# Kernel tuning notes

Measured on AMD Instinct MI355X. Metric: run time of the kernel, lower is better.

## Reference

```python
import jax, jax.numpy as jnp
import numpy as np
from jax import lax

B0 = 64
WIN, STEP, WSIZE, NCH, T = 5, 50, 100, 59, 300
EPS = 1e-5


def _bn(y, g, b, axes):
    mu = y.mean(axis=axes, keepdims=True)
    var = y.var(axis=axes, keepdims=True)
    return (y - mu) * lax.rsqrt(var + EPS) * g + b


def _conv_block(x, w, b, g, be, pad):
    # Conv2d(1->20, (1,kw), padding='same') + BN + LeakyReLU + AvgPool(1,2)
    y = lax.conv_general_dilated(x, w, (1, 1), [(0, 0), (pad, pad)],
                                 dimension_numbers=('NCHW', 'OIHW', 'NCHW'))
    y = y + b[None, :, None, None]
    y = _bn(y, g[None, :, None, None], be[None, :, None, None], (0, 2, 3))
    y = jax.nn.leaky_relu(y, 0.01)
    n, c, h, w_ = y.shape
    return y[..., :(w_ // 2) * 2].reshape(n, c, h, w_ // 2, 2).mean(-1)


def _lstm(xs, Wih, Whh, bih, bhh):
    # torch LSTM gate order: i, f, g, o
    Bn, H = xs.shape[0], Whh.shape[1]
    bb = bih + bhh

    def step(carry, xt):
        h, c = carry
        gates = xt @ Wih.T + h @ Whh.T + bb
        i, f, g, o = jnp.split(gates, 4, axis=-1)
        c = jax.nn.sigmoid(f) * c + jax.nn.sigmoid(i) * jnp.tanh(g)
        h = jax.nn.sigmoid(o) * jnp.tanh(c)
        return (h, c), h

    init = (jnp.zeros((Bn, H), xs.dtype), jnp.zeros((Bn, H), xs.dtype))
    (h, _), ys = lax.scan(step, init, xs.transpose(1, 0, 2))
    return ys.transpose(1, 0, 2), h


def _forward(x, w1, b1, g1, be1, w2, b2, g2, be2, w3, b3, g3, be3,
             w13, b13, g13, be13, gcn_w, gcn_b, edge_w, bn2_g, bn2_b,
             w11, b11, wih0, whh0, bih0, bhh0, wih1, whh1, bih1, bhh1,
             edge_index, batch_size):
    B = batch_size
    N = B * NCH
    # segment 300 samples into 5 overlapping windows of 100 (step 50)
    xr = x.reshape(B, NCH, -1).transpose(0, 2, 1)              # [B,T,59]
    idx = (jnp.arange(WIN) * STEP)[:, None] + jnp.arange(WSIZE)[None, :]
    seg = xr[:, idx, :]                                        # [B,5,100,59]
    xc = seg.transpose(0, 1, 3, 2).reshape(B * WIN, 1, NCH, WSIZE)
    # three parallel temporal conv branches
    x1 = _conv_block(xc, w1, b1, g1, be1, 62)
    x2 = _conv_block(xc, w2, b2, g2, be2, 29)
    x3 = _conv_block(xc, w3, b3, g3, be3, 15)
    xcat = jnp.concatenate([x1, x2, x3], axis=-1)              # [B*5,20,59,150]
    # cnn_13: 1x1 conv + BN + LeakyReLU, then channel sum
    y = jnp.einsum('nchw,oc->nohw', xcat, w13[:, :, 0, 0]) + b13[None, :, None, None]
    y = _bn(y, g13[None, :, None, None], be13[None, :, None, None], (0, 2, 3))
    y = jax.nn.leaky_relu(y, 0.01)
    feat = y.sum(axis=1).reshape(B, WIN, NCH, -1).transpose(0, 2, 1, 3).reshape(N, WIN, -1)  # [N,5,150]
    # GCNConv with relu'd learned per-edge weight, applied to all 5 windows
    row, col = edge_index[0], edge_index[1]
    ew = jnp.tile(jax.nn.relu(edge_w), B)                      # [E_total]
    h = jnp.einsum('nwf,fo->nwo', feat, gcn_w)                 # [N,5,100]
    deg = jnp.zeros((N,), h.dtype).at[col].add(ew) + 1.0       # +1 = self-loop weight
    dinv = lax.rsqrt(deg)
    nrm = dinv[row] * ew * dinv[col]
    agg = jnp.zeros_like(h).at[col].add(h[row] * nrm[:, None, None])
    agg = agg + h * (dinv * dinv)[:, None, None] + gcn_b       # self-loop + bias
    gout = _bn(agg, bn2_g, bn2_b, (0,))                        # per-window BN over nodes
    # cnn_11: Conv2d(1->10,(59,2)) + LeakyReLU + AvgPool(1,2)
    z = gout.reshape(B, NCH, WIN, -1).transpose(0, 2, 1, 3).reshape(B * WIN, 1, NCH, -1)
    y2 = lax.conv_general_dilated(z, w11, (1, 1), [(0, 0), (0, 0)],
                                  dimension_numbers=('NCHW', 'OIHW', 'NCHW'))
    y2 = jax.nn.leaky_relu(y2 + b11[None, :, None, None], 0.01)  # [B*5,10,1,99]
    n, c, hh, ww = y2.shape
    y2 = y2[..., :(ww // 2) * 2].reshape(n, c, hh, ww // 2, 2).mean(-1)
    seq = y2.reshape(B, WIN, -1)                               # [B,5,490]
    out1, _ = _lstm(seq, wih0, whh0, bih0, bhh0)
    out2, hlast = _lstm(out1, wih1, whh1, bih1, bhh1)
    attn = jax.nn.softmax(jnp.einsum('bth,bh->bt', out2, hlast), axis=1)
    return jnp.einsum('bth,bt->bh', out2, attn)                # [B,256]


def setup_inputs():
    key = jax.random.key(0)
    ks = jax.random.split(key, 24)
    B, E = B0, 216
    N = B * NCH
    x = jax.random.normal(ks[0], (N, T), jnp.float32)
    src = jax.random.randint(ks[1], (E,), 0, NCH)
    dst = jax.random.randint(ks[2], (E,), 0, NCH)
    off = (jnp.arange(B) * NCH)[:, None]
    edge_index = jnp.stack([(src[None, :] + off).reshape(-1),
                            (dst[None, :] + off).reshape(-1)]).astype(jnp.int32)
    s = 0.05
    return {
        'x': x,
        'w1': jax.random.normal(ks[3], (20, 1, 1, 125)) * s, 'b1': jnp.zeros(20), 'g1': jnp.ones(20), 'be1': jnp.zeros(20),
        'w2': jax.random.normal(ks[4], (20, 1, 1, 59)) * s, 'b2': jnp.zeros(20), 'g2': jnp.ones(20), 'be2': jnp.zeros(20),
        'w3': jax.random.normal(ks[5], (20, 1, 1, 31)) * s, 'b3': jnp.zeros(20), 'g3': jnp.ones(20), 'be3': jnp.zeros(20),
        'w13': jax.random.normal(ks[6], (10, 20, 1, 1)) * s, 'b13': jnp.zeros(10), 'g13': jnp.ones(10), 'be13': jnp.zeros(10),
        'gcn_w': jax.random.normal(ks[7], (150, 100)) * 0.08, 'gcn_b': jnp.zeros(100),
        'edge_w': jax.random.normal(ks[8], (216,)),
        'bn2_g': jnp.ones(100), 'bn2_b': jnp.zeros(100),
        'w11': jax.random.normal(ks[9], (10, 1, 59, 2)) * s, 'b11': jnp.zeros(10),
        'wih0': jax.random.normal(ks[10], (1024, 490)) * 0.04, 'whh0': jax.random.normal(ks[11], (1024, 256)) * 0.06,
        'bih0': jnp.zeros(1024), 'bhh0': jnp.zeros(1024),
        'wih1': jax.random.normal(ks[12], (1024, 256)) * 0.06, 'whh1': jax.random.normal(ks[13], (1024, 256)) * 0.06,
        'bih1': jnp.zeros(1024), 'bhh1': jnp.zeros(1024),
        'edge_index': edge_index,
        'batch_size': B,
    }


def reference(x, w1, b1, g1, be1, w2, b2, g2, be2, w3, b3, g3, be3,
              w13, b13, g13, be13, gcn_w, gcn_b, edge_w, bn2_g, bn2_b,
              w11, b11, wih0, whh0, bih0, bhh0, wih1, whh1, bih1, bhh1,
              edge_index, batch_size):
    return _forward(x, w1, b1, g1, be1, w2, b2, g2, be2, w3, b3, g3, be3,
                    w13, b13, g13, be13, gcn_w, gcn_b, edge_w, bn2_g, bn2_b,
                    w11, b11, wih0, whh0, bih0, bhh0, wih1, whh1, bih1, bhh1,
                    edge_index, batch_size)
```

## Files before the change

### kernel.cpp

```cpp
#include <hip/hip_runtime.h>
#include <math.h>

#define EPS 1e-5f

constexpr int NCH  = 59;
constexpr int T_   = 300;
constexpr int WIN  = 5;
constexpr int WSIZE= 100;
constexpr int Bb   = 64;
constexpr int NB   = Bb*WIN;
constexpr int NN   = Bb*NCH;
constexpr int EW_N = 216;
constexpr int NE   = EW_N*Bb;
constexpr int C1   = 20;
constexpr int C13  = 10;
constexpr int F150 = 150;
constexpr int F100 = 100;
constexpr int HID  = 256;
constexpr int GATES= 1024;
constexpr int NROW = NB*NCH;
constexpr int NWIN = NROW;
constexpr float CNT1  = 1888000.0f;
constexpr float CNT13 = 2832000.0f;

__device__ __forceinline__ float leaky(float v){ return v >= 0.f ? v : 0.01f*v; }
__device__ __forceinline__ float sigm(float v){ return 1.f/(1.f+expf(-v)); }

__global__ __launch_bounds__(256)
void zero_kernel(float* __restrict__ p, int n)
{
    int i = blockIdx.x*256 + threadIdx.x;
    if (i < n) p[i] = 0.f;
}

__global__ __launch_bounds__(256)
void syrk_kernel(const float* __restrict__ x, float* __restrict__ M, float* __restrict__ V)
{
    __shared__ float xs[128*100 + 16];
    const int k0 = blockIdx.x * 128;
    const int tid = threadIdx.x;
    for (int i = tid; i < 128*100; i += 256){
        int wl = i / 100, u = i - wl*100;
        int w = k0 + wl;
        float v = 0.f;
        if (w < NWIN){
            int row = w / 5, win = w - row*5;
            v = x[(size_t)row*T_ + win*50 + u];
        }
        xs[i] = v;
    }
    if (tid < 16) xs[128*100 + tid] = 0.f;
    __syncthreads();
    if (tid < 100){
        float s = 0.f;
        for (int kk = 0; kk < 128; kk++) s += xs[kk*100 + tid];
        atomicAdd(&V[tid], s);
    }
    const int i = tid >> 4, j = tid & 15;
    float acc[7][7];
    #pragma unroll
    for (int a=0;a<7;a++)
        #pragma unroll
        for (int b=0;b<7;b++) acc[a][b]=0.f;
    for (int kk = 0; kk < 128; kk++){
        const float* xr = &xs[kk*100];
        float xu[7], xv[7];
        #pragma unroll
        for (int a=0;a<7;a++) xu[a] = xr[a*16 + i];
        #pragma unroll
        for (int b=0;b<7;b++) xv[b] = xr[b*16 + j];
        #pragma unroll
        for (int a=0;a<7;a++)
            #pragma unroll
            for (int b=0;b<7;b++) acc[a][b] += xu[a]*xv[b];
    }
    #pragma unroll
    for (int a=0;a<7;a++){
        int u = a*16 + i;
        if (u < 100){
            #pragma unroll
            for (int b=0;b<7;b++){
                int v = b*16 + j;
                if (v < 100) atomicAdd(&M[u*100 + v], acc[a][b]);
            }
        }
    }
}

__global__ void qprep_kernel(const float* __restrict__ M, const float* __restrict__ V,
                             float* __restrict__ Q, float* __restrict__ R)
{
    int d = threadIdx.x;
    if (d < 100){
        float s = 0.f;
        Q[d*101] = 0.f;
        for (int t = 1; t <= 100; t++){
            int u = t - 1;
            if (u + d < 100) s += M[u*100 + u + d];
            Q[d*101 + t] = s;
        }
    } else if (d == 100){
        float s = 0.f;
        R[0] = 0.f;
        for (int t = 1; t <= 100; t++){ s += V[t-1]; R[t] = s; }
    }
}

__global__ __launch_bounds__(256)
void gram_finalize(const float* __restrict__ Q, const float* __restrict__ Rg,
                   const float* __restrict__ w1, const float* __restrict__ w2, const float* __restrict__ w3,
                   const float* __restrict__ g1, const float* __restrict__ be1,
                   const float* __restrict__ g2, const float* __restrict__ be2,
                   const float* __restrict__ g3, const float* __restrict__ be3,
                   float* __restrict__ sclall, float* __restrict__ sftall)
{
    __shared__ float Qs[100*101];
    __shared__ float ws[128];
    __shared__ float Rs[104];
    __shared__ float red[8];
    const int conv = blockIdx.x / 20, c = blockIdx.x - conv*20;
    const int KW  = conv==0 ? 125 : (conv==1 ? 59 : 31);
    const int PAD = (KW-1)/2;
    const float* wt = conv==0 ? w1 : (conv==1 ? w2 : w3);
    const int tid = threadIdx.x;
    for (int i = tid; i < 100*101; i += 256) Qs[i] = Q[i];
    for (int i = tid; i < KW; i += 256) ws[i] = wt[c*KW + i];
    if (tid < 101) Rs[tid] = Rg[tid];
    __syncthreads();
    const int DMAX = KW < 100 ? KW : 100;
    float sq = 0.f;
    for (int d = 0; d < DMAX; d++){
        float fac = (d == 0) ? 1.f : 2.f;
        for (int k1 = tid; k1 < KW - d; k1 += 256){
            int lo = k1 - PAD; if (lo < 0) lo = 0;
            int hi = 100 - d; int h2 = 100 + k1 - PAD; if (h2 < hi) hi = h2;
            if (hi > lo) sq += fac * ws[k1]*ws[k1+d] * (Qs[d*101 + hi] - Qs[d*101 + lo]);
        }
    }
    float sm = 0.f;
    for (int k = tid; k < KW; k += 256){
        int lo = k - PAD; if (lo < 0) lo = 0;
        int hi = 100; int h2 = k - PAD + 100; if (h2 < hi) hi = h2;
        if (hi > lo) sm += ws[k]*(Rs[hi] - Rs[lo]);
    }
    for (int off = 32; off; off >>= 1){
        sq += __shfl_down(sq, off, 64);
        sm += __shfl_down(sm, off, 64);
    }
    int wave = tid >> 6, lane = tid & 63;
    if (lane == 0){ red[wave] = sq; red[4+wave] = sm; }
    __syncthreads();
    if (tid == 0){
        float q = (red[0]+red[1]+red[2]+red[3]) / CNT1;
        float m = (red[4]+red[5]+red[6]+red[7]) / CNT1;
        float var = q - m*m;
        float rs = rsqrtf(var + EPS);
        const float* g  = conv==0 ? g1  : (conv==1 ? g2  : g3);
        const float* be = conv==0 ? be1 : (conv==1 ? be2 : be3);
        sclall[conv*C1 + c] = rs*g[c];
        sftall[conv*C1 + c] = be[c] - m*rs*g[c];
    }
}

template<int KW, int PAD, int CIDX>
__global__ __launch_bounds__(256)
void conv1d_apply(const float* __restrict__ x, const float* __restrict__ wt_g,
                  const float* __restrict__ sclall, const float* __restrict__ sftall,
                  const float* __restrict__ w13,
                  float* __restrict__ stats13, float* __restrict__ y13)
{
    __shared__ float xp[WIN*240];
    __shared__ float lstat[2*C13];

    const int row = blockIdx.x;
    const int b   = row / NCH, hh = row - b*NCH;
    const int tid = threadIdx.x;
    const float* xrow = x + (size_t)row*T_;

    for (int i = tid; i < WIN*240; i += 256){
        int win = i/240, ii = i - win*240;
        int t = ii - PAD;
        xp[i] = (t >= 0 && t < WSIZE) ? xrow[win*50 + t] : 0.f;
    }
    if (tid < 2*C13) lstat[tid] = 0.f;
    __syncthreads();

    const bool active = (tid < 250);
    const int win = tid / 50, u = tid - win*50;

    float a0[C1], a1[C1];
    #pragma unroll
    for (int c = 0; c < C1; c++){ a0[c] = 0.f; a1[c] = 0.f; }

    if (active){
        const float* xw = &xp[win*240 + 2*u];
        float xa = xw[0];
        #pragma unroll 4
        for (int k = 0; k < KW; k++){
            float xb = xw[k+1];
            #pragma unroll
            for (int c = 0; c < C1; c++){
                float wv = wt_g[c*KW + k];
                a0[c] += wv*xa;
                a1[c] += wv*xb;
            }
            xa = xb;
        }
    }

    float y[C13];
    if (active){
        float pooled[C1];
        #pragma unroll
        for (int c = 0; c < C1; c++){
            float sc = sclall[CIDX*C1 + c];
            float sf = sftall[CIDX*C1 + c];
            pooled[c] = 0.5f*(leaky(a0[c]*sc + sf) + leaky(a1[c]*sc + sf));
        }
        #pragma unroll
        for (int o = 0; o < C13; o++){
            float acc = 0.f;
            #pragma unroll
            for (int c = 0; c < C1; c++) acc += w13[o*C1 + c]*pooled[c];
            y[o] = acc;
        }
        const int n = b*WIN + win;
        #pragma unroll
        for (int o = 0; o < C13; o++)
            y13[(((size_t)n*C13 + o)*NCH + hh)*F150 + CIDX*50 + u] = y[o];
    } else {
        #pragma unroll
        for (int o = 0; o < C13; o++) y[o] = 0.f;
    }
    #pragma unroll
    for (int o = 0; o < C13; o++){
        float s = y[o], q = y[o]*y[o];
        for (int off = 32; off; off >>= 1){
            s += __shfl_down(s, off, 64);
            q += __shfl_down(q, off, 64);
        }
        if ((tid & 63) == 0){
            atomicAdd(&lstat[o],       s);
            atomicAdd(&lstat[C13 + o], q);
        }
    }
    __syncthreads();
    const int st = row & 63;
    if (tid < 2*C13) atomicAdd(&stats13[st*(2*C13) + tid], lstat[tid]);
}

__global__ void finalize_bn13(const float* __restrict__ stats13,
                              const float* __restrict__ g13, const float* __restrict__ be13,
                              float* __restrict__ scl13, float* __restrict__ sft13)
{
    int o = threadIdx.x;
    if (o >= C13) return;
    float s=0.f, q=0.f;
    for (int st=0; st<64; st++){
        s += stats13[st*20 + o];
        q += stats13[st*20 + C13 + o];
    }
    float m = s/CNT13, v = q/CNT13 - m*m;
    float rs = rsqrtf(v + EPS);
    scl13[o] = rs*g13[o];
    sft13[o] = be13[o] - m*rs*g13[o];
}

__global__ __launch_bounds__(256)
void feat_kernel(const float* __restrict__ y13,
                 const float* __restrict__ scl13, const float* __restrict__ sft13,
                 float* __restrict__ feat)
{
    __shared__ float scl[C13], sft[C13];
    int blk = blockIdx.x;
    int n = blk / NCH, hh = blk - n*NCH;
    int b = n / WIN, win = n - b*WIN;
    int tid = threadIdx.x;
    if (tid < C13){ scl[tid] = scl13[tid]; sft[tid] = sft13[tid]; }
    __syncthreads();
    float* fr = feat + ((size_t)(b*NCH+hh)*WIN + win)*F150;
    for (int f = tid; f < F150; f += 256){
        float acc = 0.f;
        #pragma unroll
        for (int o = 0; o < C13; o++){
            float v = y13[((size_t)(n*C13+o)*NCH+hh)*F150 + f];
            acc += leaky(v*scl[o] + sft[o]);
        }
        fr[f] = acc;
    }
}

__global__ __launch_bounds__(256)
void gcn_h_kernel(const float* __restrict__ feat, const float* __restrict__ gw,
                  float* __restrict__ h)
{
    __shared__ float fr[8*F150];
    int r0 = blockIdx.x*8;
    int tid = threadIdx.x;
    for (int i = tid; i < 8*F150; i += 256) fr[i] = feat[(size_t)r0*F150 + i];
    __syncthreads();
    for (int idx = tid; idx < 8*F100; idx += 256){
        int rr = idx / F100, j = idx - rr*F100;
        float acc = 0.f;
        const float* f = &fr[rr*F150];
        for (int k = 0; k < F150; k++) acc += f[k]*gw[k*F100 + j];
        h[(size_t)(r0+rr)*F100 + j] = acc;
    }
}

__global__ void deg_kernel(const int* __restrict__ ei, const float* __restrict__ ew,
                           float* __restrict__ deg)
{
    int e = blockIdx.x*blockDim.x + threadIdx.x;
    if (e >= NE) return;
    int c = ei[NE + e];
    float w = ew[e % EW_N]; w = w > 0.f ? w : 0.f;
    atomicAdd(&deg[c], w);
}

__global__ void dinv_kernel(float* __restrict__ deg)
{
    int i = blockIdx.x*blockDim.x + threadIdx.x;
    if (i < NN) deg[i] = rsqrtf(deg[i] + 1.0f);
}

__global__ __launch_bounds__(64)
void agg_kernel(const int* __restrict__ ei, const float* __restrict__ ew,
                const float* __restrict__ dinv, const float* __restrict__ h,
                float* __restrict__ agg)
{
    int e = blockIdx.x;
    int r = ei[e], c = ei[NE + e];
    float w = ew[e % EW_N]; w = w > 0.f ? w : 0.f;
    float nrm = dinv[r]*w*dinv[c];
    const float* hr = h + (size_t)r*(WIN*F100);
    float* ac = agg + (size_t)c*(WIN*F100);
    for (int i = threadIdx.x; i < WIN*F100; i += 64)
        atomicAdd(&ac[i], hr[i]*nrm);
}

__global__ __launch_bounds__(256)
void bn2_stats_kernel(const float* __restrict__ h, const float* __restrict__ dinv,
                      float* __restrict__ agg, float* __restrict__ s2sum, float* __restrict__ s2sq)
{
    int tid = threadIdx.x;
    int c0 = tid, c1 = tid + 256;
    float s0=0.f,q0=0.f,s1=0.f,q1=0.f;
    for (int rr = 0; rr < NCH; rr++){
        int node = blockIdx.x*NCH + rr;
        float d = dinv[node]; float d2 = d*d;
        const float* hr = h + (size_t)node*(WIN*F100);
        float* ar = agg + (size_t)node*(WIN*F100);
        float v0 = ar[c0] + hr[c0]*d2;
        ar[c0] = v0; s0 += v0; q0 += v0*v0;
        if (c1 < WIN*F100){
            float v1 = ar[c1] + hr[c1]*d2;
            ar[c1] = v1; s1 += v1; q1 += v1*v1;
        }
    }
    atomicAdd(&s2sum[c0], s0); atomicAdd(&s2sq[c0], q0);
    if (c1 < WIN*F100){ atomicAdd(&s2sum[c1], s1); atomicAdd(&s2sq[c1], q1); }
}

__global__ void bn2_fin_kernel(const float* __restrict__ s2sum, const float* __restrict__ s2sq,
                               const float* __restrict__ g2, const float* __restrict__ b2,
                               float* __restrict__ scl2, float* __restrict__ sft2)
{
    int c = blockIdx.x*blockDim.x + threadIdx.x;
    if (c >= WIN*F100) return;
    int f = c % F100;
    float m = s2sum[c]/(float)NN;
    float v = s2sq[c]/(float)NN - m*m;
    float rs = rsqrtf(v + EPS);
    scl2[c] = rs*g2[f];
    sft2[c] = b2[f] - m*rs*g2[f];
}

__global__ __launch_bounds__(256)
void zconv_kernel(const float* __restrict__ agg,
                  const float* __restrict__ scl2, const float* __restrict__ sft2,
                  const float* __restrict__ w11, const float* __restrict__ b11,
                  float* __restrict__ seq)
{
    __shared__ float z[NCH*WSIZE];
    __shared__ float ws[C13*NCH*2];
    __shared__ float sc[WSIZE], sf[WSIZE];
    int n = blockIdx.x;
    int b = n / WIN, win = n - b*WIN;
    int tid = threadIdx.x;
    if (tid < WSIZE){ sc[tid] = scl2[win*F100 + tid]; sf[tid] = sft2[win*F100 + tid]; }
    for (int i = tid; i < C13*NCH*2; i += 256) ws[i] = w11[i];
    __syncthreads();
    for (int i = tid; i < NCH*WSIZE; i += 256){
        int ch = i / WSIZE, t = i - ch*WSIZE;
        int node = b*NCH + ch;
        float v = agg[(size_t)node*(WIN*F100) + win*F100 + t];
        z[i] = v*sc[t] + sf[t];
    }
    __syncthreads();
    float* sq = seq + (size_t)n*490;
    for (int idx = tid; idx < C13*49; idx += 256){
        int o = idx / 49, p = idx - o*49;
        float ve = b11[o], vo = b11[o];
        const float* wo = &ws[o*NCH*2];
        for (int ch = 0; ch < NCH; ch++){
            float z0 = z[ch*WSIZE + 2*p];
            float z1 = z[ch*WSIZE + 2*p + 1];
            float z2 = z[ch*WSIZE + 2*p + 2];
            float w0 = wo[ch*2], w1 = wo[ch*2 + 1];
            ve += w0*z0 + w1*z1;
            vo += w0*z1 + w1*z2;
        }
        sq[o*49 + p] = 0.5f*(leaky(ve) + leaky(vo));
    }
}

__global__ void transpose_kernel(const float* __restrict__ src, float* __restrict__ dst, int R, int C)
{
    int idx = blockIdx.x*blockDim.x + threadIdx.x;
    if (idx >= R*C) return;
    int r = idx % R, c = idx / R;
    dst[idx] = src[(size_t)r*C + c];
}

__global__ __launch_bounds__(512)
void xgates_kernel(const float* __restrict__ seq, const float* __restrict__ wT,
                   const float* __restrict__ bih, const float* __restrict__ bhh,
                   float* __restrict__ xg)
{
    __shared__ float xs[16*490];
    const int rt = blockIdx.x >> 3, jt_tile = blockIdx.x & 7;
    const int r0 = rt*16, jc = jt_tile*128;
    const int tid = threadIdx.x;
    for (int i = tid; i < 16*490; i += 512)
        xs[i] = seq[(size_t)(r0 + i/490)*490 + (i - (i/490)*490)];
    __syncthreads();
    const int bl = tid >> 5, jq = tid & 31;
    const int j = jc + jq*4;
    const float* xrow = &xs[bl*490];
    float4 acc;
    {
        float4 b1v = *(const float4*)&bih[j];
        float4 b2v = *(const float4*)&bhh[j];
        acc.x = b1v.x+b2v.x; acc.y = b1v.y+b2v.y; acc.z = b1v.z+b2v.z; acc.w = b1v.w+b2v.w;
    }
    const float* wp = wT + j;
    #pragma unroll 5
    for (int k = 0; k < 490; k++){
        float xv = xrow[k];
        float4 w = *(const float4*)&wp[(size_t)k*GATES];
        acc.x += w.x*xv; acc.y += w.y*xv; acc.z += w.z*xv; acc.w += w.w*xv;
    }
    *(float4*)&xg[(size_t)(r0 + bl)*GATES + j] = acc;
}

__global__ __launch_bounds__(512)
void lstm_fused(int L,
                const float* __restrict__ xg0, const float* __restrict__ whh0T,
                const float* __restrict__ wih1T, const float* __restrict__ whh1T,
                const float* __restrict__ bih1, const float* __restrict__ bhh1,
                float* __restrict__ h0a, float* __restrict__ h0b,
                float* __restrict__ h1a, float* __restrict__ h1b,
                float* __restrict__ cs0, float* __restrict__ cs1,
                float* __restrict__ out1, float* __restrict__ out2)
{
    __shared__ float smem[16*HID*2 + 4*16*32];
    const int tid = threadIdx.x;
    if (blockIdx.x < 32){
        if (L >= WIN) return;
        const int t = L;
        const float* hin  = (t & 1) ? h0b : h0a;
        float*       hout = (t & 1) ? h0a : h0b;
        float* xs = smem;
        float* lg = smem + 16*HID;
        const int bt = blockIdx.x & 3, mt = blockIdx.x >> 2;
        const int b0 = bt*16, m0 = mt*32;
        for (int i = tid; i < 16*HID; i += 512)
            xs[i] = hin[(size_t)(b0 + (i>>8))*HID + (i&255)];
        __syncthreads();
        const int bl = tid >> 5, jq = tid & 31;
        const int g = jq >> 3, ms = (jq&7)*4;
        const int j = g*HID + m0 + ms;
        const float* xrow = &xs[bl*HID];
        float4 acc = *(const float4*)&xg0[((size_t)(b0+bl)*WIN + t)*GATES + j];
        const float* wp = whh0T + j;
        #pragma unroll 8
        for (int k = 0; k < HID; k++){
            float xv = xrow[k];
            float4 w = *(const float4*)&wp[(size_t)k*GATES];
            acc.x += w.x*xv; acc.y += w.y*xv; acc.z += w.z*xv; acc.w += w.w*xv;
        }
        *(float4*)&lg[(g*16 + bl)*32 + ms] = acc;
        __syncthreads();
        const int ib = tid >> 5, im = tid & 31;
        float gi = lg[(0*16+ib)*32+im], gf = lg[(1*16+ib)*32+im];
        float gg = lg[(2*16+ib)*32+im], go = lg[(3*16+ib)*32+im];
        const int gb = b0 + ib, gm = m0 + im;
        float c = cs0[(size_t)gb*HID + gm];
        c = sigm(gf)*c + sigm(gi)*tanhf(gg);
        float h = sigm(go)*tanhf(c);
        cs0[(size_t)gb*HID + gm] = c;
        hout[(size_t)gb*HID + gm] = h;
        out1[((size_t)gb*WIN + t)*HID + gm] = h;
    } else {
        if (L < 1) return;
        const int t = L - 1;
        const float* hin  = (t & 1) ? h1b : h1a;
        float*       hout = (t & 1) ? h1a : h1b;
        float* xs1 = smem;
        float* xs2 = smem + 16*HID;
        float* lg  = smem + 2*16*HID;
        const int blk = blockIdx.x - 32;
        const int bt = blk & 3, mt = blk >> 2;
        const int b0 = bt*16, m0 = mt*32;
        for (int i = tid; i < 16*HID; i += 512){
            xs1[i] = out1[((size_t)(b0 + (i>>8))*WIN + t)*HID + (i&255)];
            xs2[i] = hin[(size_t)(b0 + (i>>8))*HID + (i&255)];
        }
        __syncthreads();
        const int bl = tid >> 5, jq = tid & 31;
        const int g = jq >> 3, ms = (jq&7)*4;
        const int j = g*HID + m0 + ms;
        float4 acc;
        {
            float4 b1v = *(const float4*)&bih1[j];
            float4 b2v = *(const float4*)&bhh1[j];
            acc.x = b1v.x+b2v.x; acc.y = b1v.y+b2v.y; acc.z = b1v.z+b2v.z; acc.w = b1v.w+b2v.w;
        }
        const float* xrow1 = &xs1[bl*HID];
        const float* wp1 = wih1T + j;
        #pragma unroll 8
        for (int k = 0; k < HID; k++){
            float xv = xrow1[k];
            float4 w = *(const float4*)&wp1[(size_t)k*GATES];
            acc.x += w.x*xv; acc.y += w.y*xv; acc.z += w.z*xv; acc.w += w.w*xv;
        }
        const float* xrow2 = &xs2[bl*HID];
        const float* wp2 = whh1T + j;
        #pragma unroll 8
        for (int k = 0; k < HID; k++){
            float xv = xrow2[k];
            float4 w = *(const float4*)&wp2[(size_t)k*GATES];
            acc.x += w.x*xv; acc.y += w.y*xv; acc.z += w.z*xv; acc.w += w.w*xv;
        }
        *(float4*)&lg[(g*16 + bl)*32 + ms] = acc;
        __syncthreads();
        const int ib = tid >> 5, im = tid & 31;
        float gi = lg[(0*16+ib)*32+im], gf = lg[(1*16+ib)*32+im];
        float gg = lg[(2*16+ib)*32+im], go = lg[(3*16+ib)*32+im];
        const int gb = b0 + ib, gm = m0 + im;
        float c = cs1[(size_t)gb*HID + gm];
        c = sigm(gf)*c + sigm(gi)*tanhf(gg);
        float h = sigm(go)*tanhf(c);
        cs1[(size_t)gb*HID + gm] = c;
        hout[(size_t)gb*HID + gm] = h;
        out2[((size_t)gb*WIN + t)*HID + gm] = h;
    }
}

__global__ __launch_bounds__(256)
void attn_kernel(const float* __restrict__ out2, float* __restrict__ out)
{
    __shared__ float red[5*4];
    __shared__ float aw[5];
    const int b = blockIdx.x, tid = threadIdx.x;
    const float hl = out2[((size_t)b*WIN + 4)*HID + tid];
    const int wave = tid >> 6, lane = tid & 63;
    float v[5];
    #pragma unroll
    for (int t = 0; t < 5; t++){
        v[t] = out2[((size_t)b*WIN + t)*HID + tid];
        float p = v[t]*hl;
        for (int off = 32; off > 0; off >>= 1) p += __shfl_down(p, off);
        if (lane == 0) red[t*4 + wave] = p;
    }
    __syncthreads();
    if (tid == 0){
        float s[5], mx = -1e30f;
        for (int t = 0; t < 5; t++){ s[t] = red[t*4]+red[t*4+1]+red[t*4+2]+red[t*4+3]; mx = fmaxf(mx, s[t]); }
        float den = 0.f;
        for (int t = 0; t < 5; t++){ s[t] = expf(s[t]-mx); den += s[t]; }
        for (int t = 0; t < 5; t++) aw[t] = s[t]/den;
    }
    __syncthreads();
    float o = 0.f;
    #pragma unroll
    for (int t = 0; t < 5; t++) o += aw[t]*v[t];
    out[(size_t)b*HID + tid] = o;
}

extern "C" void kernel_launch(void* const* d_in, const int* in_sizes, int n_in,
                              void* d_out, int out_size, void* d_ws, size_t ws_size,
                              hipStream_t stream)
{
    const float* x     = (const float*)d_in[0];
    const float* w1    = (const float*)d_in[1];
    const float* g1    = (const float*)d_in[3];
    const float* be1   = (const float*)d_in[4];
    const float* w2    = (const float*)d_in[5];
    const float* g2    = (const float*)d_in[7];
    const float* be2   = (const float*)d_in[8];
    const float* w3    = (const float*)d_in[9];
    const float* g3    = (const float*)d_in[11];
    const float* be3   = (const float*)d_in[12];
    const float* w13   = (const float*)d_in[13];
    const float* g13   = (const float*)d_in[15];
    const float* be13  = (const float*)d_in[16];
    const float* gcn_w = (const float*)d_in[17];
    const float* edge_w= (const float*)d_in[19];
    const float* bn2g  = (const float*)d_in[20];
    const float* bn2b  = (const float*)d_in[21];
    const float* w11   = (const float*)d_in[22];
    const float* b11   = (const float*)d_in[23];
    const float* wih0  = (const float*)d_in[24];
    const float* whh0  = (const float*)d_in[25];
    const float* bih0  = (const float*)d_in[26];
    const float* bhh0  = (const float*)d_in[27];
    const float* wih1  = (const float*)d_in[28];
    const float* whh1  = (const float*)d_in[29];
    const float* bih1  = (const float*)d_in[30];
    const float* bhh1  = (const float*)d_in[31];
    const int*   ei    = (const int*)d_in[32];
    float* out = (float*)d_out;
    float* wsf = (float*)d_ws;
    (void)in_sizes; (void)n_in; (void)out_size; (void)ws_size;

    size_t off = 0;
    auto alloc = [&](size_t n){ size_t o = off; off += (n + 63) & ~(size_t)63; return o; };
    size_t Y13  = alloc((size_t)NB*C13*NCH*F150);
    size_t FEAT = alloc((size_t)NN*WIN*F150);
    size_t HB   = alloc((size_t)NN*WIN*F100);
    size_t AGG  = alloc((size_t)NN*WIN*F100);
    size_t DEG  = alloc(NN);
    size_t ST13 = alloc(64*20);
    size_t BN2S = alloc(1000);
    size_t H0A  = alloc(Bb*HID);
    size_t H0B  = alloc(Bb*HID);
    size_t H1A  = alloc(Bb*HID);
    size_t H1B  = alloc(Bb*HID);
    size_t CS0  = alloc(Bb*HID);
    size_t CS1  = alloc(Bb*HID);
    size_t MB   = alloc(100*100);
    size_t VB   = alloc(128);
    size_t SCLA = alloc(64);
    size_t SFTA = alloc(64);
    size_t QB   = alloc(100*101);
    size_t RB   = alloc(128);
    size_t SC13 = alloc(16);
    size_t SF13 = alloc(16);
    size_t SCL2 = alloc(1024);
    size_t WT0I = alloc((size_t)490*1024);
    size_t WT0H = alloc((size_t)256*1024);
    size_t WT1I = alloc((size_t)256*1024);
    size_t WT1H = alloc((size_t)256*1024);
    size_t SEQ  = alloc((size_t)Bb*WIN*490);
    size_t XG0  = alloc((size_t)NB*GATES);
    size_t OUT1 = alloc((size_t)NB*HID);
    size_t OUT2 = alloc((size_t)NB*HID);

    float* y13   = wsf + Y13;
    float* feat  = wsf + FEAT;
    float* hbuf  = wsf + HB;
    float* agg   = wsf + AGG;
    float* dinv  = wsf + DEG;
    float* st13  = wsf + ST13;
    float* bn2s  = wsf + BN2S;
    float* h0a   = wsf + H0A;
    float* h0b   = wsf + H0B;
    float* h1a   = wsf + H1A;
    float* h1b   = wsf + H1B;
    float* cs0   = wsf + CS0;
    float* cs1   = wsf + CS1;
    float* Mbuf  = wsf + MB;
    float* Vbuf  = wsf + VB;
    float* sclA  = wsf + SCLA;
    float* sftA  = wsf + SFTA;
    float* Qbuf  = wsf + QB;
    float* Rbuf  = wsf + RB;
    float* sc13  = wsf + SC13;
    float* sf13  = wsf + SF13;
    float* scl2  = wsf + SCL2;
    float* wT0i  = wsf + WT0I;
    float* wT0h  = wsf + WT0H;
    float* wT1i  = wsf + WT1I;
    float* wT1h  = wsf + WT1H;
    float* seqb  = wsf + SEQ;
    float* xg0   = wsf + XG0;
    float* out1b = wsf + OUT1;
    float* out2b = wsf + OUT2;

    int nzero = (int)(SCLA - AGG);
    zero_kernel<<<(nzero+255)/256,256,0,stream>>>(wsf + AGG, nzero);

    {
        int n0 = 1024*490;
        transpose_kernel<<<(n0+255)/256,256,0,stream>>>(wih0, wT0i, 1024, 490);
        int n1 = 1024*256;
        transpose_kernel<<<(n1+255)/256,256,0,stream>>>(whh0, wT0h, 1024, 256);
        transpose_kernel<<<(n1+255)/256,256,0,stream>>>(wih1, wT1i, 1024, 256);
        transpose_kernel<<<(n1+255)/256,256,0,stream>>>(whh1, wT1h, 1024, 256);
    }

    syrk_kernel<<<(NWIN+127)/128,256,0,stream>>>(x, Mbuf, Vbuf);
    qprep_kernel<<<1,128,0,stream>>>(Mbuf, Vbuf, Qbuf, Rbuf);
    gram_finalize<<<60,256,0,stream>>>(Qbuf, Rbuf, w1, w2, w3,
                                       g1, be1, g2, be2, g3, be3, sclA, sftA);

    conv1d_apply<125,62,0><<<NN,256,0,stream>>>(x, w1, sclA, sftA, w13, st13, y13);
    conv1d_apply< 59,29,1><<<NN,256,0,stream>>>(x, w2, sclA, sftA, w13, st13, y13);
    conv1d_apply< 31,15,2><<<NN,256,0,stream>>>(x, w3, sclA, sftA, w13, st13, y13);
    finalize_bn13<<<1,16,0,stream>>>(st13, g13, be13, sc13, sf13);

    feat_kernel<<<NROW,256,0,stream>>>(y13, sc13, sf13, feat);
    gcn_h_kernel<<<NROW/8,256,0,stream>>>(feat, gcn_w, hbuf);

    deg_kernel<<<(NE+255)/256,256,0,stream>>>(ei, edge_w, dinv);
    dinv_kernel<<<(NN+255)/256,256,0,stream>>>(dinv);
    agg_kernel<<<NE,64,0,stream>>>(ei, edge_w, dinv, hbuf, agg);
    bn2_stats_kernel<<<Bb,256,0,stream>>>(hbuf, dinv, agg, bn2s, bn2s+500);
    bn2_fin_kernel<<<2,256,0,stream>>>(bn2s, bn2s+500, bn2g, bn2b, scl2, scl2+500);

    zconv_kernel<<<NB,256,0,stream>>>(agg, scl2, scl2+500, w11, b11, seqb);

    xgates_kernel<<<160,512,0,stream>>>(seqb, wT0i, bih0, bhh0, xg0);
    for (int L = 0; L <= WIN; L++){
        lstm_fused<<<64,512,0,stream>>>(L, xg0, wT0h, wT1i, wT1h, bih1, bhh1,
                                        h0a, h0b, h1a, h1b, cs0, cs1, out1b, out2b);
    }
    attn_kernel<<<Bb,256,0,stream>>>(out2b, out);
}
```

Measured before the change: 885.5 us.

## Register-block conv to four outputs per thread, fuse feat into GCN, widen bn2 grid

The conv kernels now have each block process two rows, and each thread computes four conv outputs (two pooled outputs) using a sliding float4 window in registers. This reuses each weight load across more outputs and halves the number of blocks. The feat computation is fused into the GCN linear kernel so the intermediate feature buffer is never written to or read from global memory. The bn2 stats kernel is split over more blocks (16 nodes each) for more parallelism, at the cost of more atomic partial sums. The float4 loads assume 16-byte alignment of the shared buffer offsets, and the extra accumulators raise register pressure.

After: 809.3 us. -8.6%, faster.

```diff
diff --git a/kernel.cpp b/kernel.cpp
--- a/kernel.cpp
+++ b/kernel.cpp
@@ -164,89 +164,125 @@
 
 template<int KW, int PAD, int CIDX>
 __global__ __launch_bounds__(256)
-void conv1d_apply(const float* __restrict__ x, const float* __restrict__ wt_g,
-                  const float* __restrict__ sclall, const float* __restrict__ sftall,
-                  const float* __restrict__ w13,
-                  float* __restrict__ stats13, float* __restrict__ y13)
-{
-    __shared__ float xp[WIN*240];
-    __shared__ float lstat[2*C13];
-
-    const int row = blockIdx.x;
-    const int b   = row / NCH, hh = row - b*NCH;
+void conv1d_apply4(const float* __restrict__ x, const float* __restrict__ wt_g,
+                   const float* __restrict__ sclall, const float* __restrict__ sftall,
+                   const float* __restrict__ w13,
+                   float* __restrict__ stats13, float* __restrict__ y13)
+{
+    __shared__ float xp[2*WIN*240];
+    __shared__ float lstat[2][2*C13];
+
+    const int row0 = blockIdx.x*2;
     const int tid = threadIdx.x;
-    const float* xrow = x + (size_t)row*T_;
-
-    for (int i = tid; i < WIN*240; i += 256){
-        int win = i/240, ii = i - win*240;
-        int t = ii - PAD;
-        xp[i] = (t >= 0 && t < WSIZE) ? xrow[win*50 + t] : 0.f;
-    }
-    if (tid < 2*C13) lstat[tid] = 0.f;
-    __syncthreads();
-
-    const bool active = (tid < 250);
-    const int win = tid / 50, u = tid - win*50;
-
-    float a0[C1], a1[C1];
+    const int half = tid >> 7;
+    const int t2 = tid & 127;
+    const int row = row0 + half;
+    const int b = row / NCH, hh = row - b*NCH;
+
+    for (int i = tid; i < 2*WIN*240; i += 256){
+        int rr = i / 1200, ii = i - rr*1200;
+        int win = ii/240, jj = ii - win*240;
+        int t = jj - PAD;
+        xp[i] = (t >= 0 && t < WSIZE) ? x[(size_t)(row0+rr)*T_ + win*50 + t] : 0.f;
+    }
+    if (t2 < 2*C13) lstat[half][t2] = 0.f;
+    __syncthreads();
+
+    const bool active = (t2 < 125);
+    const int win = t2/25, q = t2 - win*25;
+
+    float a[C1][4];
     #pragma unroll
-    for (int c = 0; c < C1; c++){ a0[c] = 0.f; a1[c] = 0.f; }
+    for (int c = 0; c < C1; c++){ a[c][0]=0.f; a[c][1]=0.f; a[c][2]=0.f; a[c][3]=0.f; }
 
     if (active){
-        const float* xw = &xp[win*240 + 2*u];
-        float xa = xw[0];
-        #pragma unroll 4
-        for (int k = 0; k < KW; k++){
-            float xb = xw[k+1];
+        const float* xw = &xp[half*1200 + win*240 + 4*q];
+        float xv[8];
+        #pragma unroll
+        for (int i = 0; i < 4; i++) xv[i] = xw[i];
+        constexpr int KB = KW/4;
+        for (int kb = 0; kb < KB; kb++){
+            float4 nx = *(const float4*)&xw[kb*4 + 4];
+            xv[4]=nx.x; xv[5]=nx.y; xv[6]=nx.z; xv[7]=nx.w;
             #pragma unroll
-            for (int c = 0; c < C1; c++){
-                float wv = wt_g[c*KW + k];
-                a0[c] += wv*xa;
-                a1[c] += wv*xb;
+            for (int j = 0; j < 4; j++){
+                const int k = kb*4 + j;
+                #pragma unroll
+                for (int c = 0; c < C1; c++){
+                    float wv = wt_g[c*KW + k];
+                    a[c][0] += wv*xv[j];
+                    a[c][1] += wv*xv[j+1];
+                    a[c][2] += wv*xv[j+2];
+                    a[c][3] += wv*xv[j+3];
+                }
             }
-            xa = xb;
-        }
-    }
-
-    float y[C13];
+            xv[0]=xv[4]; xv[1]=xv[5]; xv[2]=xv[6]; xv[3]=xv[7];
+        }
+        constexpr int KT = KW - KB*4;
+        if (KT > 0){
+            float4 nx = *(const float4*)&xw[KB*4 + 4];
+            xv[4]=nx.x; xv[5]=nx.y; xv[6]=nx.z; xv[7]=nx.w;
+            #pragma unroll
+            for (int jt = 0; jt < KT; jt++){
+                const int k = KB*4 + jt;
+                #pragma unroll
+                for (int c = 0; c < C1; c++){
+                    float wv = wt_g[c*KW + k];
+                    a[c][0] += wv*xv[jt];
+                    a[c][1] += wv*xv[jt+1];
+                    a[c][2] += wv*xv[jt+2];
+                    a[c][3] += wv*xv[jt+3];
+                }
+            }
+        }
+    }
+
+    float y[C13][2];
     if (active){
-        float pooled[C1];
+        float pooled[C1][2];
         #pragma unroll
         for (int c = 0; c < C1; c++){
             float sc = sclall[CIDX*C1 + c];
             float sf = sftall[CIDX*C1 + c];
-            pooled[c] = 0.5f*(leaky(a0[c]*sc + sf) + leaky(a1[c]*sc + sf));
+            pooled[c][0] = 0.5f*(leaky(a[c][0]*sc + sf) + leaky(a[c][1]*sc + sf));
+            pooled[c][1] = 0.5f*(leaky(a[c][2]*sc + sf) + leaky(a[c][3]*sc + sf));
         }
         #pragma unroll
         for (int o = 0; o < C13; o++){
-            float acc = 0.f;
+            float acc0 = 0.f, acc1 = 0.f;
             #pragma unroll
-            for (int c = 0; c < C1; c++) acc += w13[o*C1 + c]*pooled[c];
-            y[o] = acc;
+            for (int c = 0; c < C1; c++){
+                float wv = w13[o*C1 + c];
+                acc0 += wv*pooled[c][0];
+                acc1 += wv*pooled[c][1];
+            }
+            y[o][0] = acc0; y[o][1] = acc1;
         }
         const int n = b*WIN + win;
         #pragma unroll
-        for (int o = 0; o < C13; o++)
-            y13[(((size_t)n*C13 + o)*NCH + hh)*F150 + CIDX*50 + u] = y[o];
+        for (int o = 0; o < C13; o++){
+            float2 st2 = make_float2(y[o][0], y[o][1]);
+            *(float2*)&y13[(((size_t)n*C13 + o)*NCH + hh)*F150 + CIDX*50 + 2*q] = st2;
+        }
     } else {
         #pragma unroll
-        for (int o = 0; o < C13; o++) y[o] = 0.f;
+        for (int o = 0; o < C13; o++){ y[o][0]=0.f; y[o][1]=0.f; }
     }
     #pragma unroll
     for (int o = 0; o < C13; o++){
-        float s = y[o], q = y[o]*y[o];
+        float s = y[o][0] + y[o][1];
+        float qq = y[o][0]*y[o][0] + y[o][1]*y[o][1];
         for (int off = 32; off; off >>= 1){
-            s += __shfl_down(s, off, 64);
-            q += __shfl_down(q, off, 64);
+            s  += __shfl_down(s,  off, 64);
+            qq += __shfl_down(qq, off, 64);
         }
         if ((tid & 63) == 0){
-            atomicAdd(&lstat[o],       s);
-            atomicAdd(&lstat[C13 + o], q);
-        }
-    }
-    __syncthreads();
-    const int st = row & 63;
-    if (tid < 2*C13) atomicAdd(&stats13[st*(2*C13) + tid], lstat[tid]);
+            atomicAdd(&lstat[half][o],       s);
+            atomicAdd(&lstat[half][C13 + o], qq);
+        }
+    }
+    __syncthreads();
+    if (t2 < 2*C13) atomicAdd(&stats13[(row & 63)*(2*C13) + t2], lstat[half][t2]);
 }
 
 __global__ void finalize_bn13(const float* __restrict__ stats13,
@@ -267,37 +303,31 @@
 }
 
 __global__ __launch_bounds__(256)
-void feat_kernel(const float* __restrict__ y13,
-                 const float* __restrict__ scl13, const float* __restrict__ sft13,
-                 float* __restrict__ feat)
-{
+void feat_gcn_kernel(const float* __restrict__ y13,
+                     const float* __restrict__ scl13, const float* __restrict__ sft13,
+                     const float* __restrict__ gw,
+                     float* __restrict__ h)
+{
+    __shared__ float fr[8*F150];
     __shared__ float scl[C13], sft[C13];
-    int blk = blockIdx.x;
-    int n = blk / NCH, hh = blk - n*NCH;
-    int b = n / WIN, win = n - b*WIN;
-    int tid = threadIdx.x;
+    const int r0 = blockIdx.x*8;
+    const int tid = threadIdx.x;
     if (tid < C13){ scl[tid] = scl13[tid]; sft[tid] = sft13[tid]; }
     __syncthreads();
-    float* fr = feat + ((size_t)(b*NCH+hh)*WIN + win)*F150;
-    for (int f = tid; f < F150; f += 256){
+    for (int i = tid; i < 8*F150; i += 256){
+        int rr = i/F150, f = i - rr*F150;
+        int r = r0 + rr;
+        int bq = r/(NCH*WIN), rem = r - bq*(NCH*WIN);
+        int hh = rem/WIN, win = rem - hh*WIN;
+        int n = bq*WIN + win;
         float acc = 0.f;
         #pragma unroll
         for (int o = 0; o < C13; o++){
-            float v = y13[((size_t)(n*C13+o)*NCH+hh)*F150 + f];
+            float v = y13[(((size_t)n*C13 + o)*NCH + hh)*F150 + f];
             acc += leaky(v*scl[o] + sft[o]);
         }
-        fr[f] = acc;
-    }
-}
-
-__global__ __launch_bounds__(256)
-void gcn_h_kernel(const float* __restrict__ feat, const float* __restrict__ gw,
-                  float* __restrict__ h)
-{
-    __shared__ float fr[8*F150];
-    int r0 = blockIdx.x*8;
-    int tid = threadIdx.x;
-    for (int i = tid; i < 8*F150; i += 256) fr[i] = feat[(size_t)r0*F150 + i];
+        fr[i] = acc;
+    }
     __syncthreads();
     for (int idx = tid; idx < 8*F100; idx += 256){
         int rr = idx / F100, j = idx - rr*F100;
@@ -346,8 +376,8 @@
     int tid = threadIdx.x;
     int c0 = tid, c1 = tid + 256;
     float s0=0.f,q0=0.f,s1=0.f,q1=0.f;
-    for (int rr = 0; rr < NCH; rr++){
-        int node = blockIdx.x*NCH + rr;
+    for (int rr = 0; rr < 16; rr++){
+        int node = blockIdx.x*16 + rr;
         float d = dinv[node]; float d2 = d*d;
         const float* hr = h + (size_t)node*(WIN*F100);
         float* ar = agg + (size_t)node*(WIN*F100);
@@ -628,7 +658,6 @@
     size_t off = 0;
     auto alloc = [&](size_t n){ size_t o = off; off += (n + 63) & ~(size_t)63; return o; };
     size_t Y13  = alloc((size_t)NB*C13*NCH*F150);
-    size_t FEAT = alloc((size_t)NN*WIN*F150);
     size_t HB   = alloc((size_t)NN*WIN*F100);
     size_t AGG  = alloc((size_t)NN*WIN*F100);
     size_t DEG  = alloc(NN);
@@ -659,7 +688,6 @@
     size_t OUT2 = alloc((size_t)NB*HID);
 
     float* y13   = wsf + Y13;
-    float* feat  = wsf + FEAT;
     float* hbuf  = wsf + HB;
     float* agg   = wsf + AGG;
     float* dinv  = wsf + DEG;
@@ -706,18 +734,17 @@
     gram_finalize<<<60,256,0,stream>>>(Qbuf, Rbuf, w1, w2, w3,
                                        g1, be1, g2, be2, g3, be3, sclA, sftA);
 
-    conv1d_apply<125,62,0><<<NN,256,0,stream>>>(x, w1, sclA, sftA, w13, st13, y13);
-    conv1d_apply< 59,29,1><<<NN,256,0,stream>>>(x, w2, sclA, sftA, w13, st13, y13);
-    conv1d_apply< 31,15,2><<<NN,256,0,stream>>>(x, w3, sclA, sftA, w13, st13, y13);
+    conv1d_apply4<125,62,0><<<NN/2,256,0,stream>>>(x, w1, sclA, sftA, w13, st13, y13);
+    conv1d_apply4< 59,29,1><<<NN/2,256,0,stream>>>(x, w2, sclA, sftA, w13, st13, y13);
+    conv1d_apply4< 31,15,2><<<NN/2,256,0,stream>>>(x, w3, sclA, sftA, w13, st13, y13);
     finalize_bn13<<<1,16,0,stream>>>(st13, g13, be13, sc13, sf13);
 
-    feat_kernel<<<NROW,256,0,stream>>>(y13, sc13, sf13, feat);
-    gcn_h_kernel<<<NROW/8,256,0,stream>>>(feat, gcn_w, hbuf);
+    feat_gcn_kernel<<<NROW/8,256,0,stream>>>(y13, sc13, sf13, gcn_w, hbuf);
 
     deg_kernel<<<(NE+255)/256,256,0,stream>>>(ei, edge_w, dinv);
     dinv_kernel<<<(NN+255)/256,256,0,stream>>>(dinv);
     agg_kernel<<<NE,64,0,stream>>>(ei, edge_w, dinv, hbuf, agg);
-    bn2_stats_kernel<<<Bb,256,0,stream>>>(hbuf, dinv, agg, bn2s, bn2s+500);
+    bn2_stats_kernel<<<NN/16,256,0,stream>>>(hbuf, dinv, agg, bn2s, bn2s+500);
     bn2_fin_kernel<<<2,256,0,stream>>>(bn2s, bn2s+500, bn2g, bn2b, scl2, scl2+500);
 
     zconv_kernel<<<NB,256,0,stream>>>(agg, scl2, scl2+500, w11, b11, seqb);
```
